# Kernel optimization log

Measured on AMD Instinct MI355X. Metric: run time of the kernel, lower is better.

Reference implementation:

```python
import jax, jax.numpy as jnp
import numpy as np
import math

D_MODEL = 512
D_STATE = 16
D_CONV = 4
EXPAND = 2
D_INNER = EXPAND * D_MODEL          # 1024
D_HALF = D_INNER // 2               # 512
DT_RANK = math.ceil(D_MODEL / 16)   # 32
BATCH, SEQLEN = 2, 4096
DT_MIN, DT_MAX, DT_FLOOR = 0.001, 0.1, 1e-4


def setup_inputs() -> dict:
    key = jax.random.key(0)
    ks = jax.random.split(key, 9)

    def lin(k, fan_out, fan_in):
        return jax.random.normal(k, (fan_out, fan_in), jnp.float32) / np.float32(np.sqrt(fan_in))

    hidden_states = jax.random.normal(ks[0], (BATCH, SEQLEN, D_MODEL), jnp.float32)
    in_proj_w = lin(ks[1], D_INNER, D_MODEL)
    x_proj_w = lin(ks[2], DT_RANK + 2 * D_STATE, D_HALF)
    dt_std = np.float32(DT_RANK ** -0.5)
    dt_proj_w = jax.random.uniform(ks[3], (D_HALF, DT_RANK), jnp.float32, -dt_std, dt_std)
    dt = jnp.exp(jax.random.uniform(ks[4], (D_HALF,), jnp.float32)
                 * (math.log(DT_MAX) - math.log(DT_MIN)) + math.log(DT_MIN))
    dt = jnp.clip(dt, DT_FLOOR)
    dt_proj_b = dt + jnp.log(-jnp.expm1(-dt))  # inverse-softplus init
    A_log = jnp.log(jnp.tile(jnp.arange(1, D_STATE + 1, dtype=jnp.float32)[None, :], (D_HALF, 1)))
    D = jnp.ones((D_HALF,), jnp.float32)
    out_proj_w = lin(ks[5], D_MODEL, D_INNER)
    conv1d_x_w = jax.random.normal(ks[6], (D_HALF, 1, D_CONV), jnp.float32) / np.float32(np.sqrt(D_CONV))
    conv1d_z_w = jax.random.normal(ks[7], (D_HALF, 1, D_CONV), jnp.float32) / np.float32(np.sqrt(D_CONV))
    return dict(hidden_states=hidden_states, in_proj_w=in_proj_w,
                conv1d_x_w=conv1d_x_w, conv1d_z_w=conv1d_z_w,
                x_proj_w=x_proj_w, dt_proj_w=dt_proj_w, dt_proj_b=dt_proj_b,
                A_log=A_log, D=D, out_proj_w=out_proj_w)


def _dwconv_same(x, w):
    # x: (b, c, l); w: (c, 1, k) depthwise. torch padding='same' with k=4 pads (1, 2),
    # which matches lax 'SAME'.
    return jax.lax.conv_general_dilated(
        x, w, window_strides=(1,), padding='SAME',
        dimension_numbers=('NCH', 'OIH', 'NCH'),
        feature_group_count=x.shape[1])


def _selective_scan(x, delta, A, B, C, D):
    # x, delta: (b, d, l); A: (d, n); B, C: (b, n, l); D: (d,)
    dA = jnp.exp(jnp.einsum('bdl,dn->bldn', delta, A))        # (b, l, d, n)
    dBx = jnp.einsum('bdl,bnl,bdl->bldn', delta, B, x)        # (b, l, d, n)

    def combine(c1, c2):
        a1, b1 = c1
        a2, b2 = c2
        return a1 * a2, a2 * b1 + b2

    _, h = jax.lax.associative_scan(combine, (dA, dBx), axis=1)  # h: (b, l, d, n)
    y = jnp.einsum('bldn,bnl->bdl', h, C) + D[None, :, None] * x
    return y


def reference(hidden_states, in_proj_w, conv1d_x_w, conv1d_z_w, x_proj_w,
              dt_proj_w, dt_proj_b, A_log, D, out_proj_w):
    b, l, _ = hidden_states.shape
    xz = jnp.einsum('bld,ed->bel', hidden_states, in_proj_w)   # (b, d_inner, l)
    x, z = jnp.split(xz, 2, axis=1)                            # each (b, d_half, l)
    A = -jnp.exp(A_log.astype(jnp.float32))
    x = jax.nn.silu(_dwconv_same(x, conv1d_x_w))
    z = jax.nn.silu(_dwconv_same(z, conv1d_z_w))
    x_dbl = jnp.einsum('bdl,ed->bel', x, x_proj_w)             # (b, dt_rank+2n, l)
    dt_r = x_dbl[:, :DT_RANK]                                  # (b, dt_rank, l)
    Bm = x_dbl[:, DT_RANK:DT_RANK + D_STATE]                   # (b, n, l)
    Cm = x_dbl[:, DT_RANK + D_STATE:]                          # (b, n, l)
    dt = jnp.einsum('brl,dr->bdl', dt_r, dt_proj_w)            # (b, d_half, l)
    delta = jax.nn.softplus(dt + dt_proj_b.astype(jnp.float32)[None, :, None])
    y = _selective_scan(x, delta, A, Bm, Cm, D.astype(jnp.float32))
    y = jnp.concatenate([y, z], axis=1)                        # (b, d_inner, l)
    out = jnp.einsum('bdl,ed->ble', y, out_proj_w)             # (b, l, d_model)
    return out
```

## Files before the change

kernel.cpp:

```cpp
#include <hip/hip_runtime.h>
#include <math.h>

#define BB 2
#define LL 4096
#define DMODEL 512
#define DINNER 1024
#define DHALF 512
#define DSTATE 16
#define RK 32
#define NCH 64
#define NC 256
#define CLEN (LL/NC)
#define NG 16
#define GL (NC/NG)
#define LOG2E 1.44269504088896f

typedef __attribute__((ext_vector_type(8))) short short8;
typedef __attribute__((ext_vector_type(4))) float f32x4;

__device__ __forceinline__ float silu_f(float v) { return v / (1.f + __expf(-v)); }

__device__ __forceinline__ unsigned short f2bf(float x) {
    unsigned int u = __float_as_uint(x);
    u += 0x7fffu + ((u >> 16) & 1u);
    return (unsigned short)(u >> 16);
}
__device__ __forceinline__ float bf2f(unsigned short u) {
    return __uint_as_float((unsigned int)u << 16);
}

__device__ __forceinline__ float softplus_f(float x) {
    return fmaxf(x, 0.f) + __logf(1.f + __expf(-fabsf(x)));
}

__device__ __forceinline__ float exp2_raw(float x) { return __builtin_amdgcn_exp2f(x); }

__device__ __forceinline__ void gload16(const unsigned short* g, unsigned short* l) {
    __builtin_amdgcn_global_load_lds((const __attribute__((address_space(1))) void*)g,
                                     (__attribute__((address_space(3))) void*)l, 16, 0, 0);
}

#define H4  1048576
#define W14 131072
#define W24 131072
#define W34 8192
__global__ void cast_all(const float* __restrict__ hid, const float* __restrict__ w1,
                         const float* __restrict__ w2, const float* __restrict__ w3,
                         unsigned short* __restrict__ Hb, unsigned short* __restrict__ Wb,
                         unsigned short* __restrict__ Wob, unsigned short* __restrict__ Wxb) {
    int i = blockIdx.x * 256 + threadIdx.x;
    const float* src; unsigned short* dst; int j;
    if (i < H4)                    { src = hid; dst = Hb;  j = i; }
    else if (i < H4 + W14)         { src = w1;  dst = Wb;  j = i - H4; }
    else if (i < H4 + W14 + W24)   { src = w2;  dst = Wob; j = i - H4 - W14; }
    else if (i < H4 + W14 + W24 + W34) { src = w3; dst = Wxb; j = i - H4 - W14 - W24; }
    else return;
    float4 v = *(const float4*)&src[(size_t)j * 4];
    ushort4 o = make_ushort4(f2bf(v.x), f2bf(v.y), f2bf(v.z), f2bf(v.w));
    *(ushort4*)&dst[(size_t)j * 4] = o;
}

template<int K, int E, bool BF16OUT>
__global__ __launch_bounds__(256, 4) void gemm_mfma(const unsigned short* __restrict__ W,
                                                    const unsigned short* __restrict__ X,
                                                    void* __restrict__ outv) {
    __shared__ unsigned short Xa[128 * 64];
    __shared__ unsigned short Wa[64 * 64];
    const int tid = threadIdx.x;
    const int lane = tid & 63;
    const int w = tid >> 6;
    const int frow = lane & 15;
    const int kg = lane >> 4;
    const int e0 = blockIdx.y * 64;
    const int r0 = blockIdx.x * 128;

    f32x4 acc[4][2] = {};

    for (int kt = 0; kt < K / 64; ++kt) {
        #pragma unroll
        for (int i = 0; i < 4; ++i) {
            int flat = i * 256 + tid;
            int row = flat >> 3;
            int slot = flat & 7;
            int chunk = slot ^ (row & 7);
            gload16(&X[(size_t)(r0 + row) * K + kt * 64 + chunk * 8], &Xa[flat * 8]);
        }
        #pragma unroll
        for (int i = 0; i < 2; ++i) {
            int flat = i * 256 + tid;
            int row = flat >> 3;
            int slot = flat & 7;
            int chunk = slot ^ (row & 7);
            gload16(&W[(size_t)(e0 + row) * K + kt * 64 + chunk * 8], &Wa[flat * 8]);
        }
        __syncthreads();

        #pragma unroll
        for (int ks = 0; ks < 2; ++ks) {
            short8 af[4], bfr[2];
            #pragma unroll
            for (int m = 0; m < 4; ++m) {
                int row = m * 16 + frow;
                int phys = (ks * 4 + kg) ^ (row & 7);
                af[m] = *(const short8*)&Wa[row * 64 + phys * 8];
            }
            #pragma unroll
            for (int n = 0; n < 2; ++n) {
                int row = w * 32 + n * 16 + frow;
                int phys = (ks * 4 + kg) ^ (row & 7);
                bfr[n] = *(const short8*)&Xa[row * 64 + phys * 8];
            }
            #pragma unroll
            for (int m = 0; m < 4; ++m)
                #pragma unroll
                for (int n = 0; n < 2; ++n)
                    acc[m][n] = __builtin_amdgcn_mfma_f32_16x16x32_bf16(af[m], bfr[n], acc[m][n], 0, 0, 0);
        }
        __syncthreads();
    }

    #pragma unroll
    for (int m = 0; m < 4; ++m) {
        #pragma unroll
        for (int n = 0; n < 2; ++n) {
            int e = e0 + m * 16 + kg * 4;
            int r = r0 + w * 32 + n * 16 + frow;
            f32x4 a = acc[m][n];
            if constexpr (BF16OUT) {
                ushort4 o = make_ushort4(f2bf(a.x), f2bf(a.y), f2bf(a.z), f2bf(a.w));
                *(ushort4*)&((unsigned short*)outv)[(size_t)r * E + e] = o;
            } else {
                *(f32x4*)&((float*)outv)[(size_t)r * E + e] = a;
            }
        }
    }
}

__global__ __launch_bounds__(256) void gemm_xproj(const unsigned short* __restrict__ W,
                                                  const unsigned short* __restrict__ X,
                                                  float* __restrict__ out) {
    __shared__ unsigned short Xa[128 * 64];
    __shared__ unsigned short Wa[64 * 64];
    const int tid = threadIdx.x;
    const int lane = tid & 63;
    const int w = tid >> 6;
    const int frow = lane & 15;
    const int kg = lane >> 4;
    const int r0 = blockIdx.x * 128;

    f32x4 acc[4][2] = {};

    for (int kt = 0; kt < 512 / 64; ++kt) {
        #pragma unroll
        for (int i = 0; i < 4; ++i) {
            int flat = i * 256 + tid;
            int row = flat >> 3;
            int slot = flat & 7;
            int chunk = slot ^ (row & 7);
            gload16(&X[(size_t)(r0 + row) * 512 + kt * 64 + chunk * 8], &Xa[flat * 8]);
        }
        #pragma unroll
        for (int i = 0; i < 2; ++i) {
            int flat = i * 256 + tid;
            int row = flat >> 3;
            int slot = flat & 7;
            int chunk = slot ^ (row & 7);
            gload16(&W[(size_t)row * 512 + kt * 64 + chunk * 8], &Wa[flat * 8]);
        }
        __syncthreads();

        #pragma unroll
        for (int ks = 0; ks < 2; ++ks) {
            short8 af[4], bfr[2];
            #pragma unroll
            for (int m = 0; m < 4; ++m) {
                int row = m * 16 + frow;
                int phys = (ks * 4 + kg) ^ (row & 7);
                af[m] = *(const short8*)&Wa[row * 64 + phys * 8];
            }
            #pragma unroll
            for (int n = 0; n < 2; ++n) {
                int row = w * 32 + n * 16 + frow;
                int phys = (ks * 4 + kg) ^ (row & 7);
                bfr[n] = *(const short8*)&Xa[row * 64 + phys * 8];
            }
            #pragma unroll
            for (int m = 0; m < 4; ++m)
                #pragma unroll
                for (int n = 0; n < 2; ++n)
                    acc[m][n] = __builtin_amdgcn_mfma_f32_16x16x32_bf16(af[m], bfr[n], acc[m][n], 0, 0, 0);
        }
        __syncthreads();
    }

    #pragma unroll
    for (int m = 0; m < 4; ++m) {
        #pragma unroll
        for (int n = 0; n < 2; ++n) {
            int r = r0 + w * 32 + n * 16 + frow;
            int b = r >> 12;
            int l = r & (LL - 1);
            int e = m * 16 + kg * 4;
            #pragma unroll
            for (int i = 0; i < 4; ++i)
                out[((size_t)b * NCH + e + i) * LL + l] = acc[m][n][i];
        }
    }
}

__global__ void conv_silu(const unsigned short* __restrict__ xzb,
                          const float* __restrict__ wx, const float* __restrict__ wz,
                          unsigned short* __restrict__ xqb, unsigned short* __restrict__ ycb) {
    __shared__ float s[67][64];
    const int b = blockIdx.z;
    const int l0 = blockIdx.x * 64;
    const int c0 = blockIdx.y * 64;
    const int tid = threadIdx.x;
    for (int idx = tid; idx < 67 * 16; idx += 256) {
        int rr = idx >> 4, u = idx & 15;
        int l = l0 - 1 + rr;
        float4 f;
        if (l >= 0 && l < LL) {
            ushort4 v = *(const ushort4*)&xzb[((size_t)b * LL + l) * DINNER + c0 + u * 4];
            f = make_float4(bf2f(v.x), bf2f(v.y), bf2f(v.z), bf2f(v.w));
        } else f = make_float4(0.f, 0.f, 0.f, 0.f);
        *(float4*)&s[rr][u * 4] = f;
    }
    __syncthreads();
    const int ct = (tid & 15) * 4;
    const int c = c0 + ct;
    const bool isx = (c < DHALF);
    const float* wp = isx ? &wx[c * 4] : &wz[(c - DHALF) * 4];
    float4 w0 = *(const float4*)&wp[0];
    float4 w1 = *(const float4*)&wp[4];
    float4 w2 = *(const float4*)&wp[8];
    float4 w3 = *(const float4*)&wp[12];
    #pragma unroll
    for (int rep = 0; rep < 4; ++rep) {
        int ll = (tid >> 4) + rep * 16;
        float4 t0 = *(const float4*)&s[ll][ct];
        float4 t1 = *(const float4*)&s[ll + 1][ct];
        float4 t2 = *(const float4*)&s[ll + 2][ct];
        float4 t3 = *(const float4*)&s[ll + 3][ct];
        float v0 = w0.x*t0.x + w0.y*t1.x + w0.z*t2.x + w0.w*t3.x;
        float v1 = w1.x*t0.y + w1.y*t1.y + w1.z*t2.y + w1.w*t3.y;
        float v2 = w2.x*t0.z + w2.y*t1.z + w2.z*t2.z + w2.w*t3.z;
        float v3 = w3.x*t0.w + w3.y*t1.w + w3.z*t2.w + w3.w*t3.w;
        ushort4 o = make_ushort4(f2bf(silu_f(v0)), f2bf(silu_f(v1)),
                                 f2bf(silu_f(v2)), f2bf(silu_f(v3)));
        int l = l0 + ll;
        if (isx) *(ushort4*)&xqb[((size_t)b * LL + l) * DHALF + c] = o;
        else     *(ushort4*)&ycb[((size_t)b * LL + l) * DINNER + c] = o;
    }
}

__global__ __launch_bounds__(256, 4) void scan1(const unsigned short* __restrict__ xqb,
                      const float* __restrict__ xdbl, const float* __restrict__ A_log,
                      const float* __restrict__ dtw, const float* __restrict__ dtb,
                      float* __restrict__ sdelb, float* __restrict__ hend) {
    __shared__ float s[48][CLEN];
    const int b = blockIdx.z;
    const int d = blockIdx.y * 256 + threadIdx.x;
    const int c = blockIdx.x;
    const int tid = threadIdx.x;
    for (int idx = tid; idx < 48 * CLEN; idx += 256) {
        int ch = idx >> 4, ll = idx & (CLEN - 1);
        s[ch][ll] = xdbl[((size_t)b * NCH + ch) * LL + c * CLEN + ll];
    }
    float dtwreg[RK];
    #pragma unroll
    for (int r = 0; r < RK; r += 4) {
        float4 v = *(const float4*)&dtw[d * RK + r];
        dtwreg[r] = v.x; dtwreg[r+1] = v.y; dtwreg[r+2] = v.z; dtwreg[r+3] = v.w;
    }
    float Arow2[DSTATE];
    #pragma unroll
    for (int n = 0; n < DSTATE; ++n) Arow2[n] = -expf(A_log[d * DSTATE + n]) * LOG2E;
    const float bias = dtb[d];
    float del[CLEN];
    #pragma unroll
    for (int t = 0; t < CLEN; ++t) del[t] = bias;
    __syncthreads();
    #pragma unroll
    for (int r = 0; r < RK; ++r) {
        float wv = dtwreg[r];
        #pragma unroll
        for (int q = 0; q < CLEN / 4; ++q) {
            float4 v = *(const float4*)&s[r][q * 4];
            del[q*4+0] = fmaf(v.x, wv, del[q*4+0]);
            del[q*4+1] = fmaf(v.y, wv, del[q*4+1]);
            del[q*4+2] = fmaf(v.z, wv, del[q*4+2]);
            del[q*4+3] = fmaf(v.w, wv, del[q*4+3]);
        }
    }
    float sdel = 0.f;
    #pragma unroll
    for (int t = 0; t < CLEN; ++t) { del[t] = softplus_f(del[t]); sdel += del[t]; }

    float h[DSTATE];
    #pragma unroll
    for (int n = 0; n < DSTATE; ++n) h[n] = 0.f;
    #pragma unroll
    for (int t = 0; t < CLEN; ++t) {
        float dl = del[t];
        float xv = bf2f(xqb[((size_t)b * LL + c * CLEN + t) * DHALF + d]);
        float dx = dl * xv;
        #pragma unroll
        for (int n = 0; n < DSTATE; ++n) {
            float dA = exp2_raw(dl * Arow2[n]);
            h[n] = fmaf(dA, h[n], dx * s[32 + n][t]);
        }
    }
    sdelb[((size_t)b * NC + c) * DHALF + d] = sdel;
    size_t base = (((size_t)b * NC + c) * DSTATE) * DHALF + d;
    #pragma unroll
    for (int n = 0; n < DSTATE; ++n)
        hend[base + (size_t)n * DHALF] = h[n];
}

__global__ void scan2a(const float* __restrict__ sdelb, float* __restrict__ hend,
                       const float* __restrict__ A_log,
                       float* __restrict__ gP, float* __restrict__ gH) {
    int flat = blockIdx.x * 256 + threadIdx.x;
    int d = flat & (DHALF - 1);
    int n = (flat >> 9) & (DSTATE - 1);
    int g = (flat >> 13) & (NG - 1);
    int b = flat >> 17;
    const float Arow2 = -expf(A_log[d * DSTATE + n]) * LOG2E;
    const size_t stride = (size_t)DSTATE * DHALF;
    size_t idx = (((size_t)b * NC + g * GL) * DSTATE + n) * DHALF + d;
    size_t sidx = ((size_t)b * NC + g * GL) * DHALF + d;
    float S = 0.f, H = 0.f;
    #pragma unroll
    for (int j = 0; j < GL; ++j) {
        float sd = sdelb[sidx + (size_t)j * DHALF];
        float h = hend[idx];
        hend[idx] = H;
        H = fmaf(exp2_raw(Arow2 * sd), H, h);
        S += sd;
        idx += stride;
    }
    size_t gi = (((size_t)b * NG + g) * DSTATE + n) * DHALF + d;
    gP[gi] = exp2_raw(Arow2 * S);
    gH[gi] = H;
}

__global__ void scan2b(const float* __restrict__ gP, float* __restrict__ gH) {
    int flat = blockIdx.x * 256 + threadIdx.x;
    int d = flat & (DHALF - 1);
    int n = (flat >> 9) & (DSTATE - 1);
    int b = flat >> 13;
    float h = 0.f;
    const size_t stride = (size_t)DSTATE * DHALF;
    size_t gi = (((size_t)b * NG) * DSTATE + n) * DHALF + d;
    for (int g = 0; g < NG; ++g) {
        float P = gP[gi], Hh = gH[gi];
        gH[gi] = h;
        h = fmaf(P, h, Hh);
        gi += stride;
    }
}

__global__ __launch_bounds__(256, 4) void scan3(const unsigned short* __restrict__ xqb,
                      const float* __restrict__ xdbl, const float* __restrict__ A_log,
                      const float* __restrict__ dtw, const float* __restrict__ dtb,
                      const float* __restrict__ Dp, const float* __restrict__ sdelb,
                      const float* __restrict__ hend, const float* __restrict__ gH,
                      unsigned short* __restrict__ ycb) {
    __shared__ float s[64][CLEN];
    const int b = blockIdx.z;
    const int d = blockIdx.y * 256 + threadIdx.x;
    const int c = blockIdx.x;
    const int tid = threadIdx.x;
    for (int idx = tid; idx < 64 * CLEN; idx += 256) {
        int ch = idx >> 4, ll = idx & (CLEN - 1);
        s[ch][ll] = xdbl[((size_t)b * NCH + ch) * LL + c * CLEN + ll];
    }
    float Sc = 0.f;
    {
        const int g0 = (c / GL) * GL;
        for (int j = g0; j < c; ++j)
            Sc += sdelb[((size_t)b * NC + j) * DHALF + d];
    }
    float dtwreg[RK];
    #pragma unroll
    for (int r = 0; r < RK; r += 4) {
        float4 v = *(const float4*)&dtw[d * RK + r];
        dtwreg[r] = v.x; dtwreg[r+1] = v.y; dtwreg[r+2] = v.z; dtwreg[r+3] = v.w;
    }
    float Arow2[DSTATE], h[DSTATE];
    size_t base = (((size_t)b * NC + c) * DSTATE) * DHALF + d;
    size_t gbase = (((size_t)b * NG + (c / GL)) * DSTATE) * DHALF + d;
    #pragma unroll
    for (int n = 0; n < DSTATE; ++n) {
        Arow2[n] = -expf(A_log[d * DSTATE + n]) * LOG2E;
        h[n] = fmaf(exp2_raw(Arow2[n] * Sc), gH[gbase + (size_t)n * DHALF],
                    hend[base + (size_t)n * DHALF]);
    }
    const float bias = dtb[d];
    const float Dv = Dp[d];
    float del[CLEN];
    #pragma unroll
    for (int t = 0; t < CLEN; ++t) del[t] = bias;
    __syncthreads();
    #pragma unroll
    for (int r = 0; r < RK; ++r) {
        float wv = dtwreg[r];
        #pragma unroll
        for (int q = 0; q < CLEN / 4; ++q) {
            float4 v = *(const float4*)&s[r][q * 4];
            del[q*4+0] = fmaf(v.x, wv, del[q*4+0]);
            del[q*4+1] = fmaf(v.y, wv, del[q*4+1]);
            del[q*4+2] = fmaf(v.z, wv, del[q*4+2]);
            del[q*4+3] = fmaf(v.w, wv, del[q*4+3]);
        }
    }
    #pragma unroll
    for (int t = 0; t < CLEN; ++t) del[t] = softplus_f(del[t]);

    #pragma unroll
    for (int t = 0; t < CLEN; ++t) {
        float dl = del[t];
        float xv = bf2f(xqb[((size_t)b * LL + c * CLEN + t) * DHALF + d]);
        float dx = dl * xv;
        float y = Dv * xv;
        #pragma unroll
        for (int n = 0; n < DSTATE; ++n) {
            float dA = exp2_raw(dl * Arow2[n]);
            h[n] = fmaf(dA, h[n], dx * s[32 + n][t]);
            y = fmaf(h[n], s[48 + n][t], y);
        }
        ycb[((size_t)b * LL + c * CLEN + t) * DINNER + d] = f2bf(y);
    }
}

extern "C" void kernel_launch(void* const* d_in, const int* in_sizes, int n_in,
                              void* d_out, int out_size, void* d_ws, size_t ws_size,
                              hipStream_t stream) {
    const float* hidden     = (const float*)d_in[0];
    const float* in_proj_w  = (const float*)d_in[1];
    const float* conv_x_w   = (const float*)d_in[2];
    const float* conv_z_w   = (const float*)d_in[3];
    const float* x_proj_w   = (const float*)d_in[4];
    const float* dt_proj_w  = (const float*)d_in[5];
    const float* dt_proj_b  = (const float*)d_in[6];
    const float* A_log      = (const float*)d_in[7];
    const float* Dp         = (const float*)d_in[8];
    const float* out_proj_w = (const float*)d_in[9];
    float* out = (float*)d_out;

    float* ws_f = (float*)d_ws;
    unsigned short* Wb  = (unsigned short*)(ws_f + 0);
    unsigned short* Wob = (unsigned short*)(ws_f + 262144);
    unsigned short* Wxb = (unsigned short*)(ws_f + 524288);
    unsigned short* Hb  = (unsigned short*)(ws_f + 540672);
    unsigned short* xzb = (unsigned short*)(ws_f + 2637824);
    unsigned short* xqb = (unsigned short*)(ws_f + 6832128);
    unsigned short* ycb = (unsigned short*)(ws_f + 8929280);
    float* xdbl = ws_f + 13123584;
    float* gP   = ws_f + 13647872;
    float* gH   = ws_f + 13910016;
    float* sdel = ws_f + 540672;
    float* hend = ws_f + 2637824;

    dim3 blk(256);

    cast_all<<<dim3((H4 + W14 + W24 + W34 + 255) / 256), blk, 0, stream>>>(
        hidden, in_proj_w, out_proj_w, x_proj_w, Hb, Wb, Wob, Wxb);
    gemm_mfma<DMODEL, DINNER, true><<<dim3(BB * LL / 128, DINNER / 64), blk, 0, stream>>>(Wb, Hb, xzb);
    conv_silu<<<dim3(LL / 64, DINNER / 64, BB), blk, 0, stream>>>(xzb, conv_x_w, conv_z_w, xqb, ycb);
    gemm_xproj<<<dim3(BB * LL / 128), blk, 0, stream>>>(Wxb, xqb, xdbl);
    scan1<<<dim3(NC, DHALF / 256, BB), blk, 0, stream>>>(xqb, xdbl, A_log, dt_proj_w, dt_proj_b, sdel, hend);
    scan2a<<<dim3(BB * NG * DSTATE * DHALF / 256), blk, 0, stream>>>(sdel, hend, A_log, gP, gH);
    scan2b<<<dim3(BB * DSTATE * DHALF / 256), blk, 0, stream>>>(gP, gH);
    scan3<<<dim3(NC, DHALF / 256, BB), blk, 0, stream>>>(xqb, xdbl, A_log, dt_proj_w, dt_proj_b,
                                                         Dp, sdel, hend, gH, ycb);
    gemm_mfma<DINNER, DMODEL, false><<<dim3(BB * LL / 128, DMODEL / 64), blk, 0, stream>>>(Wob, ycb, out);
}
```

Measured before the change: 130.0 us.

## Store delta from scan1, fold group carry into scan3, precompute scaled A

scan1 now writes the softplus delta values to a workspace buffer, so scan3 reads them instead of recomputing the dt projection and softplus. The separate scan2b kernel is removed, and each scan3 block instead recomputes the cross-group carry by looping over preceding group prefixes. The -exp(A_log)*log2e table is computed once in cast_all and stored transposed. This trades recomputation and one launch for extra global traffic (a 16 MB delta buffer written and read) and redundant per-block carry loops of up to 15 groups.

```diff
diff --git a/kernel.cpp b/kernel.cpp
--- a/kernel.cpp
+++ b/kernel.cpp
@@ -44,17 +44,27 @@
 #define W14 131072
 #define W24 131072
 #define W34 8192
+#define NA  8192
 __global__ void cast_all(const float* __restrict__ hid, const float* __restrict__ w1,
                          const float* __restrict__ w2, const float* __restrict__ w3,
+                         const float* __restrict__ A_log,
                          unsigned short* __restrict__ Hb, unsigned short* __restrict__ Wb,
-                         unsigned short* __restrict__ Wob, unsigned short* __restrict__ Wxb) {
+                         unsigned short* __restrict__ Wob, unsigned short* __restrict__ Wxb,
+                         float* __restrict__ Arow2T) {
     int i = blockIdx.x * 256 + threadIdx.x;
+    if (i >= H4 + W14 + W24 + W34) {
+        int j = i - (H4 + W14 + W24 + W34);
+        if (j < NA) {
+            int n = j >> 9, d = j & 511;
+            Arow2T[j] = -expf(A_log[d * DSTATE + n]) * LOG2E;
+        }
+        return;
+    }
     const float* src; unsigned short* dst; int j;
     if (i < H4)                    { src = hid; dst = Hb;  j = i; }
     else if (i < H4 + W14)         { src = w1;  dst = Wb;  j = i - H4; }
     else if (i < H4 + W14 + W24)   { src = w2;  dst = Wob; j = i - H4 - W14; }
-    else if (i < H4 + W14 + W24 + W34) { src = w3; dst = Wxb; j = i - H4 - W14 - W24; }
-    else return;
+    else                           { src = w3;  dst = Wxb; j = i - H4 - W14 - W24; }
     float4 v = *(const float4*)&src[(size_t)j * 4];
     ushort4 o = make_ushort4(f2bf(v.x), f2bf(v.y), f2bf(v.z), f2bf(v.w));
     *(ushort4*)&dst[(size_t)j * 4] = o;
@@ -255,9 +265,10 @@
 }
 
 __global__ __launch_bounds__(256, 4) void scan1(const unsigned short* __restrict__ xqb,
-                      const float* __restrict__ xdbl, const float* __restrict__ A_log,
+                      const float* __restrict__ xdbl, const float* __restrict__ Arow2T,
                       const float* __restrict__ dtw, const float* __restrict__ dtb,
-                      float* __restrict__ sdelb, float* __restrict__ hend) {
+                      float* __restrict__ sdelb, float* __restrict__ delb,
+                      float* __restrict__ hend) {
     __shared__ float s[48][CLEN];
     const int b = blockIdx.z;
     const int d = blockIdx.y * 256 + threadIdx.x;
@@ -275,7 +286,7 @@
     }
     float Arow2[DSTATE];
     #pragma unroll
-    for (int n = 0; n < DSTATE; ++n) Arow2[n] = -expf(A_log[d * DSTATE + n]) * LOG2E;
+    for (int n = 0; n < DSTATE; ++n) Arow2[n] = Arow2T[n * DHALF + d];
     const float bias = dtb[d];
     float del[CLEN];
     #pragma unroll
@@ -296,6 +307,9 @@
     float sdel = 0.f;
     #pragma unroll
     for (int t = 0; t < CLEN; ++t) { del[t] = softplus_f(del[t]); sdel += del[t]; }
+    size_t dbase = ((size_t)b * LL + c * CLEN) * DHALF + d;
+    #pragma unroll
+    for (int t = 0; t < CLEN; ++t) delb[dbase + (size_t)t * DHALF] = del[t];
 
     float h[DSTATE];
     #pragma unroll
@@ -319,14 +333,14 @@
 }
 
 __global__ void scan2a(const float* __restrict__ sdelb, float* __restrict__ hend,
-                       const float* __restrict__ A_log,
+                       const float* __restrict__ Arow2T,
                        float* __restrict__ gP, float* __restrict__ gH) {
     int flat = blockIdx.x * 256 + threadIdx.x;
     int d = flat & (DHALF - 1);
     int n = (flat >> 9) & (DSTATE - 1);
     int g = (flat >> 13) & (NG - 1);
     int b = flat >> 17;
-    const float Arow2 = -expf(A_log[d * DSTATE + n]) * LOG2E;
+    const float Arow2 = Arow2T[n * DHALF + d];
     const size_t stride = (size_t)DSTATE * DHALF;
     size_t idx = (((size_t)b * NC + g * GL) * DSTATE + n) * DHALF + d;
     size_t sidx = ((size_t)b * NC + g * GL) * DHALF + d;
@@ -345,79 +359,52 @@
     gH[gi] = H;
 }
 
-__global__ void scan2b(const float* __restrict__ gP, float* __restrict__ gH) {
-    int flat = blockIdx.x * 256 + threadIdx.x;
-    int d = flat & (DHALF - 1);
-    int n = (flat >> 9) & (DSTATE - 1);
-    int b = flat >> 13;
-    float h = 0.f;
-    const size_t stride = (size_t)DSTATE * DHALF;
-    size_t gi = (((size_t)b * NG) * DSTATE + n) * DHALF + d;
-    for (int g = 0; g < NG; ++g) {
-        float P = gP[gi], Hh = gH[gi];
-        gH[gi] = h;
-        h = fmaf(P, h, Hh);
-        gi += stride;
-    }
-}
-
 __global__ __launch_bounds__(256, 4) void scan3(const unsigned short* __restrict__ xqb,
-                      const float* __restrict__ xdbl, const float* __restrict__ A_log,
-                      const float* __restrict__ dtw, const float* __restrict__ dtb,
-                      const float* __restrict__ Dp, const float* __restrict__ sdelb,
-                      const float* __restrict__ hend, const float* __restrict__ gH,
+                      const float* __restrict__ xdbl, const float* __restrict__ Arow2T,
+                      const float* __restrict__ delb, const float* __restrict__ Dp,
+                      const float* __restrict__ sdelb, const float* __restrict__ hend,
+                      const float* __restrict__ gP, const float* __restrict__ gH,
                       unsigned short* __restrict__ ycb) {
-    __shared__ float s[64][CLEN];
+    __shared__ float s[32][CLEN];
     const int b = blockIdx.z;
     const int d = blockIdx.y * 256 + threadIdx.x;
     const int c = blockIdx.x;
     const int tid = threadIdx.x;
-    for (int idx = tid; idx < 64 * CLEN; idx += 256) {
-        int ch = idx >> 4, ll = idx & (CLEN - 1);
-        s[ch][ll] = xdbl[((size_t)b * NCH + ch) * LL + c * CLEN + ll];
+    const int g = c / GL;
+    for (int idx = tid; idx < 32 * CLEN; idx += 256) {
+        int ch = 32 + (idx >> 4), ll = idx & (CLEN - 1);
+        s[idx >> 4][ll] = xdbl[((size_t)b * NCH + ch) * LL + c * CLEN + ll];
+    }
+    float Arow2[DSTATE];
+    #pragma unroll
+    for (int n = 0; n < DSTATE; ++n) Arow2[n] = Arow2T[n * DHALF + d];
+
+    float Hcar[DSTATE];
+    #pragma unroll
+    for (int n = 0; n < DSTATE; ++n) Hcar[n] = 0.f;
+    for (int gp = 0; gp < g; ++gp) {
+        size_t gi = (((size_t)b * NG + gp) * DSTATE) * DHALF + d;
+        #pragma unroll
+        for (int n = 0; n < DSTATE; ++n)
+            Hcar[n] = fmaf(gP[gi + (size_t)n * DHALF], Hcar[n], gH[gi + (size_t)n * DHALF]);
     }
     float Sc = 0.f;
-    {
-        const int g0 = (c / GL) * GL;
-        for (int j = g0; j < c; ++j)
-            Sc += sdelb[((size_t)b * NC + j) * DHALF + d];
-    }
-    float dtwreg[RK];
-    #pragma unroll
-    for (int r = 0; r < RK; r += 4) {
-        float4 v = *(const float4*)&dtw[d * RK + r];
-        dtwreg[r] = v.x; dtwreg[r+1] = v.y; dtwreg[r+2] = v.z; dtwreg[r+3] = v.w;
-    }
-    float Arow2[DSTATE], h[DSTATE];
+    for (int j = g * GL; j < c; ++j)
+        Sc += sdelb[((size_t)b * NC + j) * DHALF + d];
+
+    float h[DSTATE];
     size_t base = (((size_t)b * NC + c) * DSTATE) * DHALF + d;
-    size_t gbase = (((size_t)b * NG + (c / GL)) * DSTATE) * DHALF + d;
-    #pragma unroll
-    for (int n = 0; n < DSTATE; ++n) {
-        Arow2[n] = -expf(A_log[d * DSTATE + n]) * LOG2E;
-        h[n] = fmaf(exp2_raw(Arow2[n] * Sc), gH[gbase + (size_t)n * DHALF],
-                    hend[base + (size_t)n * DHALF]);
-    }
-    const float bias = dtb[d];
+    #pragma unroll
+    for (int n = 0; n < DSTATE; ++n)
+        h[n] = fmaf(exp2_raw(Arow2[n] * Sc), Hcar[n], hend[base + (size_t)n * DHALF]);
+
+    float del[CLEN];
+    size_t dbase = ((size_t)b * LL + c * CLEN) * DHALF + d;
+    #pragma unroll
+    for (int t = 0; t < CLEN; ++t) del[t] = delb[dbase + (size_t)t * DHALF];
+
     const float Dv = Dp[d];
-    float del[CLEN];
-    #pragma unroll
-    for (int t = 0; t < CLEN; ++t) del[t] = bias;
     __syncthreads();
-    #pragma unroll
-    for (int r = 0; r < RK; ++r) {
-        float wv = dtwreg[r];
-        #pragma unroll
-        for (int q = 0; q < CLEN / 4; ++q) {
-            float4 v = *(const float4*)&s[r][q * 4];
-            del[q*4+0] = fmaf(v.x, wv, del[q*4+0]);
-            del[q*4+1] = fmaf(v.y, wv, del[q*4+1]);
-            del[q*4+2] = fmaf(v.z, wv, del[q*4+2]);
-            del[q*4+3] = fmaf(v.w, wv, del[q*4+3]);
-        }
-    }
-    #pragma unroll
-    for (int t = 0; t < CLEN; ++t) del[t] = softplus_f(del[t]);
-
     #pragma unroll
     for (int t = 0; t < CLEN; ++t) {
         float dl = del[t];
@@ -427,8 +414,8 @@
         #pragma unroll
         for (int n = 0; n < DSTATE; ++n) {
             float dA = exp2_raw(dl * Arow2[n]);
-            h[n] = fmaf(dA, h[n], dx * s[32 + n][t]);
-            y = fmaf(h[n], s[48 + n][t], y);
+            h[n] = fmaf(dA, h[n], dx * s[n][t]);
+            y = fmaf(h[n], s[16 + n][t], y);
         }
         ycb[((size_t)b * LL + c * CLEN + t) * DINNER + d] = f2bf(y);
     }
@@ -460,20 +447,22 @@
     float* xdbl = ws_f + 13123584;
     float* gP   = ws_f + 13647872;
     float* gH   = ws_f + 13910016;
+    float* Arow2T = ws_f + 14172160;
+    float* delb = ws_f + 14180352;
     float* sdel = ws_f + 540672;
     float* hend = ws_f + 2637824;
 
     dim3 blk(256);
 
-    cast_all<<<dim3((H4 + W14 + W24 + W34 + 255) / 256), blk, 0, stream>>>(
-        hidden, in_proj_w, out_proj_w, x_proj_w, Hb, Wb, Wob, Wxb);
+    cast_all<<<dim3((H4 + W14 + W24 + W34 + NA + 255) / 256), blk, 0, stream>>>(
+        hidden, in_proj_w, out_proj_w, x_proj_w, A_log, Hb, Wb, Wob, Wxb, Arow2T);
     gemm_mfma<DMODEL, DINNER, true><<<dim3(BB * LL / 128, DINNER / 64), blk, 0, stream>>>(Wb, Hb, xzb);
     conv_silu<<<dim3(LL / 64, DINNER / 64, BB), blk, 0, stream>>>(xzb, conv_x_w, conv_z_w, xqb, ycb);
     gemm_xproj<<<dim3(BB * LL / 128), blk, 0, stream>>>(Wxb, xqb, xdbl);
-    scan1<<<dim3(NC, DHALF / 256, BB), blk, 0, stream>>>(xqb, xdbl, A_log, dt_proj_w, dt_proj_b, sdel, hend);
-    scan2a<<<dim3(BB * NG * DSTATE * DHALF / 256), blk, 0, stream>>>(sdel, hend, A_log, gP, gH);
-    scan2b<<<dim3(BB * DSTATE * DHALF / 256), blk, 0, stream>>>(gP, gH);
-    scan3<<<dim3(NC, DHALF / 256, BB), blk, 0, stream>>>(xqb, xdbl, A_log, dt_proj_w, dt_proj_b,
-                                                         Dp, sdel, hend, gH, ycb);
+    scan1<<<dim3(NC, DHALF / 256, BB), blk, 0, stream>>>(xqb, xdbl, Arow2T, dt_proj_w, dt_proj_b,
+                                                         sdel, delb, hend);
+    scan2a<<<dim3(BB * NG * DSTATE * DHALF / 256), blk, 0, stream>>>(sdel, hend, Arow2T, gP, gH);
+    scan3<<<dim3(NC, DHALF / 256, BB), blk, 0, stream>>>(xqb, xdbl, Arow2T, delb, Dp,
+                                                         sdel, hend, gP, gH, ycb);
     gemm_mfma<DINNER, DMODEL, false><<<dim3(BB * LL / 128, DMODEL / 64), blk, 0, stream>>>(Wob, ycb, out);
 }
```

After: 127.5 us. About the same (-1.9%).
